# Optimization experiments

Measured on AMD Instinct MI355X. Metric: run time of the kernel, lower is better.

## Reference

```python
import jax, jax.numpy as jnp
import numpy as np

IN_FEATURES = 128
HIDDEN = 128
NUM_BAGS = 128
BAG = 8192
N = NUM_BAGS * BAG
TEMP = 1.0
# sm_alpha=0.5 -> coef = 1/(1-0.5)-1 = 1 -> iteration alpha = 1/(1+coef) = 0.5
ITER_ALPHA = 0.5


def setup_inputs() -> dict:
    key = jax.random.key(0)
    k0, k1, k2 = jax.random.split(key, 3)
    x = jax.random.normal(k0, (N, IN_FEATURES), jnp.float32)
    W1 = jax.random.normal(k1, (IN_FEATURES, HIDDEN), jnp.float32) / np.sqrt(IN_FEATURES)
    b1 = jnp.zeros((HIDDEN,), jnp.float32)
    W2 = jax.random.normal(k2, (HIDDEN, 1), jnp.float32) / np.sqrt(HIDDEN)
    b2 = jnp.zeros((1,), jnp.float32)
    lengths = jnp.full((NUM_BAGS,), BAG, jnp.int32)  # bags sum to N
    return {"x": x, "W1": W1, "b1": b1, "W2": W2, "b2": b2, "lengths": lengths}


def _smooth_step(w, same_left, same_right):
    # One ApproxSm step with row-normalized tridiagonal adjacency per bag:
    # g = (1-a)*w + a*(A @ w), a = 0.5. A row i averages {i-1, i, i+1} within the bag.
    w_l = jnp.concatenate([jnp.zeros((1,), w.dtype), w[:-1]])
    w_r = jnp.concatenate([w[1:], jnp.zeros((1,), w.dtype)])
    deg = 1.0 + same_left.astype(w.dtype) + same_right.astype(w.dtype)
    Aw = (w + jnp.where(same_left, w_l, 0.0) + jnp.where(same_right, w_r, 0.0)) / deg
    return (1.0 - ITER_ALPHA) * w + ITER_ALPHA * Aw


def reference(x, W1, b1, W2, b2, lengths):
    n = x.shape[0]
    num_bags = lengths.shape[0]
    seg_ids = jnp.repeat(jnp.arange(num_bags), lengths, total_repeat_length=n)

    # attention MLP -> per-instance logit
    logits = (jnp.tanh(x @ W1 + b1) @ W2 + b2)[:, 0] / TEMP  # [N]

    # per-bag (segment) softmax, numerically stable
    m = jax.ops.segment_max(logits, seg_ids, num_segments=num_bags)
    e = jnp.exp(logits - m[seg_ids])
    s = jax.ops.segment_sum(e, seg_ids, num_segments=num_bags)
    w = e / s[seg_ids]  # [N] attention weights per bag

    # late smoothing (ApproxSm, 1 step) on the weights
    same_left = jnp.concatenate([jnp.zeros((1,), bool), seg_ids[1:] == seg_ids[:-1]])
    same_right = jnp.concatenate([seg_ids[:-1] == seg_ids[1:], jnp.zeros((1,), bool)])
    g = _smooth_step(w, same_left, same_right)

    # renormalize per bag
    gs = jax.ops.segment_sum(g, seg_ids, num_segments=num_bags)
    g = g / (gs[seg_ids] + 1e-8)

    # weighted sum per bag -> context vectors
    ctx = jax.ops.segment_sum(g[:, None] * x, seg_ids, num_segments=num_bags)  # [B, d]
    return ctx, g[:, None]
```

## Files before the change

### kernel.cpp

```cpp
#include <hip/hip_runtime.h>

#define NROWS (128*8192)
#define D 128
#define HID 128
#define NBAGS 128
#define BAG 8192

typedef __bf16 bf16x8 __attribute__((ext_vector_type(8)));
typedef float  f32x16 __attribute__((ext_vector_type(16)));

__device__ inline float tanh_fast(float v){
  float a = fabsf(v);
  float e = __expf(2.0f * a);
  float r = 1.0f - 2.0f / (e + 1.0f);
  return copysignf(r, v);
}

__global__ __launch_bounds__(256) void k_logits(
    const float* __restrict__ x, const float* __restrict__ W1,
    const float* __restrict__ b1, const float* __restrict__ W2,
    const float* __restrict__ b2, float* __restrict__ logits)
{
  __shared__ __bf16 Bh[16384];
  __shared__ __bf16 Bl[16384];
  const int tid = threadIdx.x;

  for (int idx = tid; idx < 16384; idx += 256){
    int j  = idx & 7;
    int l  = (idx >> 3) & 63;
    int kk = (idx >> 9) & 7;
    int t  = idx >> 12;
    int k  = kk*16 + ((l >> 5) << 3) + j;
    int c  = t*32 + (l & 31);
    float v = W1[k*HID + c];
    __bf16 h = (__bf16)v;
    Bh[idx] = h;
    Bl[idx] = (__bf16)(v - (float)h);
  }
  __syncthreads();

  const int lane  = tid & 63;
  const int wave  = tid >> 6;
  const int gwave = blockIdx.x * 4 + wave;
  const int nwv   = gridDim.x * 4;

  float w2v[4], b1v[4];
  #pragma unroll
  for (int t = 0; t < 4; ++t){
    w2v[t] = W2[t*32 + (lane & 31)];
    b1v[t] = b1[t*32 + (lane & 31)];
  }
  const float b2v = b2[0];

  const int rowl = lane & 31;
  const int kgrp = lane >> 5;

  for (int tile = gwave; tile < NROWS/32; tile += nwv){
    const float* xr = x + (size_t)(tile*32 + rowl) * D + kgrp*8;

    float4 u0[8], u1[8];
    #pragma unroll
    for (int kk = 0; kk < 8; ++kk){
      u0[kk] = *(const float4*)(xr + kk*16);
      u1[kk] = *(const float4*)(xr + kk*16 + 4);
    }

    f32x16 acc[4];
    #pragma unroll
    for (int t = 0; t < 4; ++t) acc[t] = (f32x16)(0.0f);

    #pragma unroll
    for (int kk = 0; kk < 8; ++kk){
      float f[8] = {u0[kk].x, u0[kk].y, u0[kk].z, u0[kk].w,
                    u1[kk].x, u1[kk].y, u1[kk].z, u1[kk].w};
      bf16x8 ah, al;
      #pragma unroll
      for (int j = 0; j < 8; ++j){
        __bf16 h = (__bf16)f[j];
        ah[j] = h;
        al[j] = (__bf16)(f[j] - (float)h);
      }
      #pragma unroll
      for (int t = 0; t < 4; ++t){
        int base = ((t*8 + kk)*64 + lane)*8;
        bf16x8 bh = *reinterpret_cast<const bf16x8*>(&Bh[base]);
        bf16x8 bl = *reinterpret_cast<const bf16x8*>(&Bl[base]);
        acc[t] = __builtin_amdgcn_mfma_f32_32x32x16_bf16(ah, bh, acc[t], 0, 0, 0);
        acc[t] = __builtin_amdgcn_mfma_f32_32x32x16_bf16(ah, bl, acc[t], 0, 0, 0);
        acc[t] = __builtin_amdgcn_mfma_f32_32x32x16_bf16(al, bh, acc[t], 0, 0, 0);
      }
    }

    float p[16];
    #pragma unroll
    for (int q = 0; q < 16; ++q) p[q] = 0.0f;
    #pragma unroll
    for (int t = 0; t < 4; ++t){
      #pragma unroll
      for (int q = 0; q < 16; ++q){
        p[q] += tanh_fast(acc[t][q] + b1v[t]) * w2v[t];
      }
    }
    #pragma unroll
    for (int m = 1; m < 32; m <<= 1){
      #pragma unroll
      for (int q = 0; q < 16; ++q) p[q] += __shfl_xor(p[q], m);
    }
    if ((lane & 31) == 0){
      int rb = tile*32 + (kgrp << 2);
      #pragma unroll
      for (int q = 0; q < 16; ++q){
        int row = (q & 3) + 8*(q >> 2);
        logits[rb + row] = p[q] + b2v;
      }
    }
  }
}

__global__ __launch_bounds__(256) void k_soft(float* __restrict__ g)
{
  __shared__ float lb[BAG];
  __shared__ float wb[BAG];
  const int tid = threadIdx.x;
  float* seg = g + (size_t)blockIdx.x * BAG;

  float4* lb4 = (float4*)lb;
  const float4* s4 = (const float4*)seg;
  #pragma unroll
  for (int i = 0; i < 8; ++i) lb4[i*256 + tid] = s4[i*256 + tid];
  __syncthreads();

  float m = -3.4e38f;
  #pragma unroll
  for (int i = 0; i < 32; ++i) m = fmaxf(m, lb[i*256 + tid]);
  wb[tid] = m; __syncthreads();
  for (int s = 128; s > 0; s >>= 1){
    if (tid < s) wb[tid] = fmaxf(wb[tid], wb[tid+s]);
    __syncthreads();
  }
  m = wb[0]; __syncthreads();

  float ls = 0.0f;
  #pragma unroll
  for (int i = 0; i < 32; ++i){
    float e = __expf(lb[i*256 + tid] - m);
    wb[i*256 + tid] = e;
    ls += e;
  }
  lb[tid] = ls; __syncthreads();
  for (int s = 128; s > 0; s >>= 1){
    if (tid < s) lb[tid] += lb[tid+s];
    __syncthreads();
  }
  float s_sum = lb[0]; __syncthreads();

  #pragma unroll
  for (int i = 0; i < 32; ++i) wb[i*256 + tid] = wb[i*256 + tid] / s_sum;
  __syncthreads();

  float gs = 0.0f;
  #pragma unroll
  for (int i = 0; i < 32; ++i){
    int idx = i*256 + tid;
    float w  = wb[idx];
    float wl = (idx > 0)       ? wb[idx-1] : 0.0f;
    float wr = (idx < BAG-1)   ? wb[idx+1] : 0.0f;
    float deg = 1.0f + (idx > 0 ? 1.0f : 0.0f) + (idx < BAG-1 ? 1.0f : 0.0f);
    float gg = 0.5f*w + 0.5f*(w + wl + wr)/deg;
    lb[idx] = gg;
    gs += gg;
  }
  __syncthreads();
  wb[tid] = gs; __syncthreads();
  for (int s = 128; s > 0; s >>= 1){
    if (tid < s) wb[tid] += wb[tid+s];
    __syncthreads();
  }
  float denom = wb[0] + 1e-8f;

  #pragma unroll
  for (int i = 0; i < 32; ++i){
    int idx = i*256 + tid;
    seg[idx] = lb[idx] / denom;
  }
}

__global__ __launch_bounds__(256) void k_ctx(
    const float* __restrict__ x, const float* __restrict__ g,
    float* __restrict__ ctx)
{
  __shared__ float4 red4[256];
  const int tid = threadIdx.x;
  const int fq  = tid & 31;
  const int rg  = tid >> 5;
  const int blk = blockIdx.x;
  const int bag = blk >> 3;
  const int r0  = bag*BAG + (blk & 7)*1024;
  const float4* x4 = (const float4*)x;

  float4 acc; acc.x = acc.y = acc.z = acc.w = 0.0f;
  #pragma unroll 8
  for (int it = 0; it < 128; ++it){
    int r = r0 + it*8 + rg;
    float gv = g[r];
    float4 xv = x4[(size_t)r*32 + fq];
    acc.x += gv*xv.x; acc.y += gv*xv.y; acc.z += gv*xv.z; acc.w += gv*xv.w;
  }
  red4[tid] = acc; __syncthreads();
  for (int s = 128; s >= 32; s >>= 1){
    if (tid < s){
      red4[tid].x += red4[tid+s].x;
      red4[tid].y += red4[tid+s].y;
      red4[tid].z += red4[tid+s].z;
      red4[tid].w += red4[tid+s].w;
    }
    __syncthreads();
  }
  if (tid < 32){
    float4 v = red4[tid];
    float* dst = ctx + bag*128 + fq*4;
    atomicAdd(dst + 0, v.x);
    atomicAdd(dst + 1, v.y);
    atomicAdd(dst + 2, v.z);
    atomicAdd(dst + 3, v.w);
  }
}

extern "C" void kernel_launch(void* const* d_in, const int* in_sizes, int n_in,
                              void* d_out, int out_size, void* d_ws, size_t ws_size,
                              hipStream_t stream)
{
  const float* x  = (const float*)d_in[0];
  const float* W1 = (const float*)d_in[1];
  const float* b1 = (const float*)d_in[2];
  const float* W2 = (const float*)d_in[3];
  const float* b2 = (const float*)d_in[4];

  float* out = (float*)d_out;
  float* ctx = out;
  float* g   = out + 16384;

  hipMemsetAsync(ctx, 0, 16384*sizeof(float), stream);
  k_logits<<<512, 256, 0, stream>>>(x, W1, b1, W2, b2, g);
  k_soft  <<<NBAGS, 256, 0, stream>>>(g);
  k_ctx   <<<1024, 256, 0, stream>>>(x, g, ctx);
}
```

Before: 925.8 us.

## Raise logits occupancy, restructure MFMA loop, use reciprocals, double ctx grid

The logits kernel now runs 512-thread blocks with a launch bound of 4 blocks per CU. Its loop converts x to bf16 hi/lo pairs up front and keeps one accumulator per output tile instead of four, which lowers register pressure and lets tanh overlap the next tile's MFMAs. Divisions in tanh and in the softmax/renormalisation are replaced by hardware reciprocals and multiplies. The context kernel's grid is doubled with half the rows per block, which adds more atomics per bag. The approximate rcp may shift results slightly, and the launch bound could cause register spills.

Result: slower. 1.178 ms (+27.3%).

```diff
diff --git a/kernel.cpp b/kernel.cpp
--- a/kernel.cpp
+++ b/kernel.cpp
@@ -12,11 +12,11 @@
 __device__ inline float tanh_fast(float v){
   float a = fabsf(v);
   float e = __expf(2.0f * a);
-  float r = 1.0f - 2.0f / (e + 1.0f);
+  float r = 1.0f - 2.0f * __builtin_amdgcn_rcpf(e + 1.0f);
   return copysignf(r, v);
 }
 
-__global__ __launch_bounds__(256) void k_logits(
+__global__ __launch_bounds__(512, 4) void k_logits(
     const float* __restrict__ x, const float* __restrict__ W1,
     const float* __restrict__ b1, const float* __restrict__ W2,
     const float* __restrict__ b2, float* __restrict__ logits)
@@ -25,7 +25,7 @@
   __shared__ __bf16 Bl[16384];
   const int tid = threadIdx.x;
 
-  for (int idx = tid; idx < 16384; idx += 256){
+  for (int idx = tid; idx < 16384; idx += 512){
     int j  = idx & 7;
     int l  = (idx >> 3) & 63;
     int kk = (idx >> 9) & 7;
@@ -41,8 +41,8 @@
 
   const int lane  = tid & 63;
   const int wave  = tid >> 6;
-  const int gwave = blockIdx.x * 4 + wave;
-  const int nwv   = gridDim.x * 4;
+  const int gwave = blockIdx.x * 8 + wave;
+  const int nwv   = gridDim.x * 8;
 
   float w2v[4], b1v[4];
   #pragma unroll
@@ -58,49 +58,42 @@
   for (int tile = gwave; tile < NROWS/32; tile += nwv){
     const float* xr = x + (size_t)(tile*32 + rowl) * D + kgrp*8;
 
-    float4 u0[8], u1[8];
+    bf16x8 ah[8], al[8];
     #pragma unroll
     for (int kk = 0; kk < 8; ++kk){
-      u0[kk] = *(const float4*)(xr + kk*16);
-      u1[kk] = *(const float4*)(xr + kk*16 + 4);
-    }
-
-    f32x16 acc[4];
-    #pragma unroll
-    for (int t = 0; t < 4; ++t) acc[t] = (f32x16)(0.0f);
-
-    #pragma unroll
-    for (int kk = 0; kk < 8; ++kk){
-      float f[8] = {u0[kk].x, u0[kk].y, u0[kk].z, u0[kk].w,
-                    u1[kk].x, u1[kk].y, u1[kk].z, u1[kk].w};
-      bf16x8 ah, al;
+      float4 a0 = *(const float4*)(xr + kk*16);
+      float4 a1 = *(const float4*)(xr + kk*16 + 4);
+      float f[8] = {a0.x, a0.y, a0.z, a0.w, a1.x, a1.y, a1.z, a1.w};
       #pragma unroll
       for (int j = 0; j < 8; ++j){
         __bf16 h = (__bf16)f[j];
-        ah[j] = h;
-        al[j] = (__bf16)(f[j] - (float)h);
-      }
-      #pragma unroll
-      for (int t = 0; t < 4; ++t){
+        ah[kk][j] = h;
+        al[kk][j] = (__bf16)(f[j] - (float)h);
+      }
+    }
+
+    float p[16];
+    #pragma unroll
+    for (int q = 0; q < 16; ++q) p[q] = 0.0f;
+
+    #pragma unroll
+    for (int t = 0; t < 4; ++t){
+      f32x16 acc = (f32x16)(0.0f);
+      #pragma unroll
+      for (int kk = 0; kk < 8; ++kk){
         int base = ((t*8 + kk)*64 + lane)*8;
         bf16x8 bh = *reinterpret_cast<const bf16x8*>(&Bh[base]);
         bf16x8 bl = *reinterpret_cast<const bf16x8*>(&Bl[base]);
-        acc[t] = __builtin_amdgcn_mfma_f32_32x32x16_bf16(ah, bh, acc[t], 0, 0, 0);
-        acc[t] = __builtin_amdgcn_mfma_f32_32x32x16_bf16(ah, bl, acc[t], 0, 0, 0);
-        acc[t] = __builtin_amdgcn_mfma_f32_32x32x16_bf16(al, bh, acc[t], 0, 0, 0);
-      }
-    }
-
-    float p[16];
-    #pragma unroll
-    for (int q = 0; q < 16; ++q) p[q] = 0.0f;
-    #pragma unroll
-    for (int t = 0; t < 4; ++t){
+        acc = __builtin_amdgcn_mfma_f32_32x32x16_bf16(ah[kk], bh, acc, 0, 0, 0);
+        acc = __builtin_amdgcn_mfma_f32_32x32x16_bf16(ah[kk], bl, acc, 0, 0, 0);
+        acc = __builtin_amdgcn_mfma_f32_32x32x16_bf16(al[kk], bh, acc, 0, 0, 0);
+      }
       #pragma unroll
       for (int q = 0; q < 16; ++q){
-        p[q] += tanh_fast(acc[t][q] + b1v[t]) * w2v[t];
-      }
-    }
+        p[q] += tanh_fast(acc[q] + b1v[t]) * w2v[t];
+      }
+    }
+
     #pragma unroll
     for (int m = 1; m < 32; m <<= 1){
       #pragma unroll
@@ -152,10 +145,10 @@
     if (tid < s) lb[tid] += lb[tid+s];
     __syncthreads();
   }
-  float s_sum = lb[0]; __syncthreads();
-
-  #pragma unroll
-  for (int i = 0; i < 32; ++i) wb[i*256 + tid] = wb[i*256 + tid] / s_sum;
+  float s_inv = __builtin_amdgcn_rcpf(lb[0]); __syncthreads();
+
+  #pragma unroll
+  for (int i = 0; i < 32; ++i) wb[i*256 + tid] = wb[i*256 + tid] * s_inv;
   __syncthreads();
 
   float gs = 0.0f;
@@ -165,8 +158,8 @@
     float w  = wb[idx];
     float wl = (idx > 0)       ? wb[idx-1] : 0.0f;
     float wr = (idx < BAG-1)   ? wb[idx+1] : 0.0f;
-    float deg = 1.0f + (idx > 0 ? 1.0f : 0.0f) + (idx < BAG-1 ? 1.0f : 0.0f);
-    float gg = 0.5f*w + 0.5f*(w + wl + wr)/deg;
+    float rdeg = (idx > 0 && idx < BAG-1) ? 0.33333334f : 0.5f;
+    float gg = 0.5f*w + 0.5f*(w + wl + wr)*rdeg;
     lb[idx] = gg;
     gs += gg;
   }
@@ -176,12 +169,12 @@
     if (tid < s) wb[tid] += wb[tid+s];
     __syncthreads();
   }
-  float denom = wb[0] + 1e-8f;
+  float dinv = 1.0f / (wb[0] + 1e-8f);
 
   #pragma unroll
   for (int i = 0; i < 32; ++i){
     int idx = i*256 + tid;
-    seg[idx] = lb[idx] / denom;
+    seg[idx] = lb[idx] * dinv;
   }
 }
 
@@ -194,13 +187,13 @@
   const int fq  = tid & 31;
   const int rg  = tid >> 5;
   const int blk = blockIdx.x;
-  const int bag = blk >> 3;
-  const int r0  = bag*BAG + (blk & 7)*1024;
+  const int bag = blk >> 4;
+  const int r0  = bag*BAG + (blk & 15)*512;
   const float4* x4 = (const float4*)x;
 
   float4 acc; acc.x = acc.y = acc.z = acc.w = 0.0f;
   #pragma unroll 8
-  for (int it = 0; it < 128; ++it){
+  for (int it = 0; it < 64; ++it){
     int r = r0 + it*8 + rg;
     float gv = g[r];
     float4 xv = x4[(size_t)r*32 + fq];
@@ -241,7 +234,7 @@
   float* g   = out + 16384;
 
   hipMemsetAsync(ctx, 0, 16384*sizeof(float), stream);
-  k_logits<<<512, 256, 0, stream>>>(x, W1, b1, W2, b2, g);
+  k_logits<<<512, 512, 0, stream>>>(x, W1, b1, W2, b2, g);
   k_soft  <<<NBAGS, 256, 0, stream>>>(g);
-  k_ctx   <<<1024, 256, 0, stream>>>(x, g, ctx);
-}
+  k_ctx   <<<2048, 256, 0, stream>>>(x, g, ctx);
+}
```
